# Kernel tuning notes

Measured on AMD Instinct MI355X. Metric: run time of the kernel, lower is better.

Reference implementation:

```python
import jax, jax.numpy as jnp
import numpy as np

B, N, S = 8, 8192, 1024
K = 16          # max_degree
HIDDEN = 192    # hidden_dim, divisible by 2*ndim -> no padding in sincos embed
NDIM = 3
MAX_WAVELENGTH = 10000.0


def sincos_embed(coords, dim, ndim):
    # Continuous sin/cos embedding: dim//ndim channels per coordinate,
    # half sin / half cos, geometric frequencies (UPT-style).
    dpw = dim // ndim                          # dims per coordinate (even)
    ar = jnp.arange(0, dpw, 2, dtype=coords.dtype)
    omega = 1.0 / (MAX_WAVELENGTH ** (ar / dpw))   # (dpw/2,)
    out = coords[..., None] * omega            # (..., ndim, dpw/2)
    emb = jnp.concatenate([jnp.sin(out), jnp.cos(out)], axis=-1)  # (..., ndim, dpw)
    return emb.reshape(*coords.shape[:-1], dim)


def knn_gather(x, sidx, k):
    # x: (B,N,ndim), sidx: (B,S) -> (B,S,k,ndim) coords of k nearest neighbors.
    # Equivalent to the original dense NxN dists[sidx] + argsort[:, :k],
    # but only computes the S rows that are used and uses top_k.
    def per_sample(sx, si):
        sp = sx[si]                                            # (S, ndim)
        d = jnp.sum((sp[:, None, :] - sx[None, :, :]) ** 2, -1)  # (S, N)
        _, nbr = jax.lax.top_k(-d, k)                          # k smallest dists
        return sx[nbr]                                         # (S, k, ndim)
    return jax.vmap(per_sample)(x, sidx)


def setup_inputs() -> dict:
    key = jax.random.key(0)
    ks = jax.random.split(key, 6)
    scale = 0.02
    return {
        "input_points": jax.random.normal(ks[0], (B, N, NDIM), dtype=jnp.float32),
        "supernode_idxs": jax.random.randint(ks[1], (B, S), 0, N),
        "w_in": jax.random.normal(ks[2], (NDIM, HIDDEN), dtype=jnp.float32) * scale,
        "b_in": jnp.zeros((HIDDEN,), dtype=jnp.float32),
        "w1": jax.random.normal(ks[3], (HIDDEN, HIDDEN), dtype=jnp.float32) * scale,
        "b1": jnp.zeros((HIDDEN,), dtype=jnp.float32),
        "w2": jax.random.normal(ks[4], (HIDDEN, HIDDEN), dtype=jnp.float32) * scale,
        "b2": jnp.zeros((HIDDEN,), dtype=jnp.float32),
    }


def reference(input_points, supernode_idxs, w_in, b_in, w1, b1, w2, b2):
    nbr = knn_gather(input_points, supernode_idxs, K)      # (B,S,K,3)
    # input projection + continuous sincos positional embedding
    h = nbr @ w_in + b_in + sincos_embed(nbr, HIDDEN, NDIM)  # (B,S,K,H)
    # message net: Dense -> gelu -> Dense
    h = jax.nn.gelu(h @ w1 + b1)
    h = h @ w2 + b2
    # mean-pool over neighbors per supernode
    return jnp.mean(h, axis=-2)                            # (B,S,H)
```

## Files before the change

kernel.cpp:

```cpp
#include <hip/hip_runtime.h>
#include <stdint.h>

#define NB   8
#define NPTS 8192
#define NS   1024
#define NK   16
#define NH   192
#define KP1  224
#define HROW 232
#define HALF 4096

typedef float    f32x4 __attribute__((ext_vector_type(4)));
typedef short    s16x8 __attribute__((ext_vector_type(8)));
typedef uint32_t u32;
typedef unsigned long long u64;

static __device__ const float OMEGA[32] = {
  1.0f, 0.74989420933245585f, 0.56234132519034907f, 0.42169650342858223f,
  0.31622776601683794f, 0.23713737056616552f, 0.17782794100389229f, 0.13335214321633237f,
  0.1f, 0.074989420933245585f, 0.056234132519034907f, 0.042169650342858223f,
  0.031622776601683794f, 0.023713737056616552f, 0.017782794100389229f, 0.013335214321633237f,
  0.01f, 0.0074989420933245585f, 0.0056234132519034907f, 0.0042169650342858223f,
  0.0031622776601683794f, 0.0023713737056616552f, 0.0017782794100389229f, 0.0013335214321633237f,
  0.001f, 0.00074989420933245585f, 0.00056234132519034907f, 0.00042169650342858223f,
  0.00031622776601683794f, 0.00023713737056616552f, 0.00017782794100389229f, 0.00013335214321633237f };

__device__ __forceinline__ uint16_t f2bf(float f) {
  u32 u = __float_as_uint(f);
  return (uint16_t)((u + 0x7FFFu + ((u >> 16) & 1u)) >> 16);
}

__global__ void __launch_bounds__(64) prep_weights(
    const float* __restrict__ w_in, const float* __restrict__ b_in,
    const float* __restrict__ w1, const float* __restrict__ b1,
    const float* __restrict__ w2,
    uint16_t* __restrict__ wT1e, uint16_t* __restrict__ wT2) {
  const int n = blockIdx.x, t = threadIdx.x;
  float p0 = 0, p1 = 0, p2 = 0, pb = 0;
  #pragma unroll
  for (int kk = 0; kk < 3; ++kk) {
    int c = kk * 64 + t;
    float w1cn = w1[c * NH + n];
    wT1e[n * KP1 + c] = f2bf(w1cn);
    wT2 [n * NH  + c] = f2bf(w2[c * NH + n]);
    p0 = fmaf(w_in[0 * NH + c], w1cn, p0);
    p1 = fmaf(w_in[1 * NH + c], w1cn, p1);
    p2 = fmaf(w_in[2 * NH + c], w1cn, p2);
    pb = fmaf(b_in[c], w1cn, pb);
  }
  #pragma unroll
  for (int off = 32; off; off >>= 1) {
    p0 += __shfl_down(p0, off);
    p1 += __shfl_down(p1, off);
    p2 += __shfl_down(p2, off);
    pb += __shfl_down(pb, off);
  }
  if (t == 0) {
    wT1e[n * KP1 + 192] = f2bf(p0);
    wT1e[n * KP1 + 193] = f2bf(p1);
    wT1e[n * KP1 + 194] = f2bf(p2);
    wT1e[n * KP1 + 195] = f2bf(pb + b1[n]);
  }
  if (t >= 4 && t < 32) wT1e[n * KP1 + 192 + t] = 0;
}

__global__ void __launch_bounds__(512) knn_kernel(const float* __restrict__ pts,
                                                  const int* __restrict__ sidx,
                                                  u64* __restrict__ keys) {
  __shared__ float2 XY[HALF];
  __shared__ float  Zs[HALF];
  const int bid = blockIdx.x;
  const int b = bid >> 6;
  const int chunk = (bid >> 1) & 31;
  const int half = bid & 1;
  const int pbase = half * HALF;
  const float* pb = pts + ((size_t)b * NPTS + pbase) * 3;
  for (int i = threadIdx.x; i < HALF; i += 512) {
    XY[i] = float2{pb[3 * i], pb[3 * i + 1]};
    Zs[i] = pb[3 * i + 2];
  }
  __syncthreads();
  const int wave = threadIdx.x >> 6, lane = threadIdx.x & 63;
  const int sbase = chunk * 32 + wave * 4;

  float sx[4], sy[4], sz[4], minD[4], Td[4];
  u32 minI[4];
  u64 arr[4], T[4];
  #pragma unroll
  for (int q = 0; q < 4; ++q) {
    int si = sidx[b * NS + sbase + q];
    const float* qp = pts + ((size_t)b * NPTS + si) * 3;
    sx[q] = qp[0]; sy[q] = qp[1]; sz[q] = qp[2];
    minD[q] = __uint_as_float(0x7F800000u);
    minI[q] = 0xFFFFFFFFu;
  }

  for (int t = 0; t < HALF / 64; ++t) {
    int lj = t * 64 + lane;
    float2 xy = XY[lj];
    float z = Zs[lj];
    #pragma unroll
    for (int q = 0; q < 4; ++q) {
      float dx = xy.x - sx[q], dy = xy.y - sy[q], dz = z - sz[q];
      float d = __fadd_rn(__fadd_rn(__fmul_rn(dx, dx), __fmul_rn(dy, dy)),
                          __fmul_rn(dz, dz));
      bool c = d < minD[q];
      minD[q] = c ? d : minD[q];
      minI[q] = c ? (u32)(pbase + lj) : minI[q];
    }
  }

  #pragma unroll
  for (int q = 0; q < 4; ++q) {
    u64 key = ((u64)__float_as_uint(minD[q]) << 32) | minI[q];
    #pragma unroll
    for (int k = 2; k <= 64; k <<= 1) {
      #pragma unroll
      for (int jj = k >> 1; jj > 0; jj >>= 1) {
        u64 p = __shfl_xor(key, jj);
        bool up      = ((lane & k) == 0);
        bool lower   = ((lane & jj) == 0);
        bool takeMin = (lower == up);
        bool pLess   = p < key;
        key = (takeMin == pLess) ? p : key;
      }
    }
    arr[q] = (lane < 16) ? key : ~0ull;
    T[q] = __shfl(key, 15);
    Td[q] = __uint_as_float((u32)(T[q] >> 32));
  }

  for (int t = 0; t < HALF / 64; ++t) {
    int lj = t * 64 + lane;
    float2 xy = XY[lj];
    float z = Zs[lj];
    #pragma unroll
    for (int q = 0; q < 4; ++q) {
      float dx = xy.x - sx[q], dy = xy.y - sy[q], dz = z - sz[q];
      float d = __fadd_rn(__fadd_rn(__fmul_rn(dx, dx), __fmul_rn(dy, dy)),
                          __fmul_rn(dz, dz));
      u64 ball = __ballot(d <= Td[q] && (u32)(pbase + lj) != minI[q]);
      if (ball) {
        u64 key = ((u64)__float_as_uint(d) << 32) | (u32)(pbase + lj);
        do {
          int src = __builtin_ctzll(ball);
          ball &= ball - 1;
          u64 k2 = __shfl(key, src);
          if (k2 < T[q]) {
            int r = __popcll(__ballot(arr[q] < k2));
            u64 up = __shfl_up(arr[q], 1);
            if (lane == r) arr[q] = k2;
            else if (lane > r && lane < 16) arr[q] = up;
            T[q] = __shfl(arr[q], 15);
            Td[q] = __uint_as_float((u32)(T[q] >> 32));
          }
        } while (ball);
      }
    }
  }
  #pragma unroll
  for (int q = 0; q < 4; ++q)
    if (lane < 16)
      keys[((size_t)(b * NS + sbase + q)) * 32 + half * 16 + lane] = arr[q];
}

__device__ __forceinline__ float h0ch(int c, const float crd[3]) {
  if (c >= 196) return 0.0f;
  if (c == 195) return 1.0f;
  if (c >= 192) return crd[c - 192];
  int dd = c >> 6, i = c & 63, m = i & 31;
  float arg = crd[dd] * OMEGA[m];
  return (i < 32) ? __sinf(arg) : __cosf(arg);
}

__device__ __forceinline__ float gelu_tanh(float x) {
  float u = 0.7978845608028654f * __fmaf_rn(0.044715f * x, x * x, x);
  float t = 1.0f - 2.0f / (__expf(2.0f * u) + 1.0f);
  return 0.5f * x * (1.0f + t);
}

__global__ void __launch_bounds__(256) mlp_kernel(
    const float* __restrict__ pts, const u64* __restrict__ keys,
    const float* __restrict__ b2v,
    const uint16_t* __restrict__ wT1e, const uint16_t* __restrict__ wT2,
    float* __restrict__ out) {
  __shared__ uint16_t hbuf[128 * HROW];
  __shared__ int nbrL[128];
  const int g = blockIdx.x, tid = threadIdx.x;
  const int wave = tid >> 6, lane = tid & 63;
  const int lrow = lane & 15, lg = lane >> 4;

  {
    int qq = tid >> 5;
    u64 k0 = keys[((size_t)g * 8 + qq) * 32 + (tid & 31)];
    int rank = 0;
    #pragma unroll
    for (int p = 0; p < 32; ++p) {
      u64 other = __shfl(k0, (lane & 32) + p);
      rank += (other < k0);
    }
    if (rank < 16) nbrL[qq * 16 + rank] = (int)(u32)k0;
  }
  __syncthreads();

  {
    int r = tid >> 1, half = tid & 1;
    int grow = g * 128 + r;
    int b = grow >> 14;
    int pidx = nbrL[r];
    const float* pp = pts + ((size_t)b * NPTS + pidx) * 3;
    float crd[3] = {pp[0], pp[1], pp[2]};
    #pragma unroll
    for (int jj = 0; jj < 56; ++jj) {
      int c = half * 112 + jj * 2;
      u32 pk = (u32)f2bf(h0ch(c, crd)) | ((u32)f2bf(h0ch(c + 1, crd)) << 16);
      *(u32*)(hbuf + r * HROW + c) = pk;
    }
  }
  __syncthreads();

  f32x4 acc1[3][8] = {};
  {
    const uint16_t* wbase = wT1e + (size_t)(wave * 48 + lrow) * KP1 + lg * 8;
    uint4 anx[3];
    #pragma unroll
    for (int nt = 0; nt < 3; ++nt) anx[nt] = *(const uint4*)(wbase + nt * 16 * KP1);
    #pragma unroll
    for (int kk = 0; kk < 7; ++kk) {
      uint4 acur[3];
      #pragma unroll
      for (int nt = 0; nt < 3; ++nt) acur[nt] = anx[nt];
      if (kk < 6) {
        #pragma unroll
        for (int nt = 0; nt < 3; ++nt)
          anx[nt] = *(const uint4*)(wbase + nt * 16 * KP1 + (kk + 1) * 32);
      }
      s16x8 bm[8];
      #pragma unroll
      for (int mt = 0; mt < 8; ++mt)
        bm[mt] = __builtin_bit_cast(s16x8,
                   *(const uint4*)(hbuf + (mt * 16 + lrow) * HROW + kk * 32 + lg * 8));
      #pragma unroll
      for (int nt = 0; nt < 3; ++nt)
        #pragma unroll
        for (int mt = 0; mt < 8; ++mt)
          acc1[nt][mt] = __builtin_amdgcn_mfma_f32_16x16x32_bf16(
              __builtin_bit_cast(s16x8, acur[nt]), bm[mt], acc1[nt][mt], 0, 0, 0);
    }
  }
  __syncthreads();

  {
    #pragma unroll
    for (int nt = 0; nt < 3; ++nt) {
      #pragma unroll
      for (int mt = 0; mt < 8; ++mt) {
        u32 lo = (u32)f2bf(gelu_tanh(acc1[nt][mt][0])) |
                 ((u32)f2bf(gelu_tanh(acc1[nt][mt][1])) << 16);
        u32 hi = (u32)f2bf(gelu_tanh(acc1[nt][mt][2])) |
                 ((u32)f2bf(gelu_tanh(acc1[nt][mt][3])) << 16);
        *(uint2*)(hbuf + (mt * 16 + lrow) * HROW + wave * 48 + nt * 16 + lg * 4) =
            uint2{lo, hi};
      }
    }
  }
  __syncthreads();

  f32x4 acc2[8][3] = {};
  {
    const uint16_t* w2base = wT2 + (size_t)(wave * 48 + lrow) * NH + lg * 8;
    uint4 bnx[3];
    #pragma unroll
    for (int nt = 0; nt < 3; ++nt) bnx[nt] = *(const uint4*)(w2base + nt * 16 * NH);
    #pragma unroll
    for (int kk = 0; kk < 6; ++kk) {
      uint4 bcur[3];
      #pragma unroll
      for (int nt = 0; nt < 3; ++nt) bcur[nt] = bnx[nt];
      if (kk < 5) {
        #pragma unroll
        for (int nt = 0; nt < 3; ++nt)
          bnx[nt] = *(const uint4*)(w2base + nt * 16 * NH + (kk + 1) * 32);
      }
      s16x8 am[8];
      #pragma unroll
      for (int mt = 0; mt < 8; ++mt)
        am[mt] = __builtin_bit_cast(s16x8,
                   *(const uint4*)(hbuf + (mt * 16 + lrow) * HROW + kk * 32 + lg * 8));
      #pragma unroll
      for (int mt = 0; mt < 8; ++mt)
        #pragma unroll
        for (int nt = 0; nt < 3; ++nt)
          acc2[mt][nt] = __builtin_amdgcn_mfma_f32_16x16x32_bf16(
              am[mt], __builtin_bit_cast(s16x8, bcur[nt]), acc2[mt][nt], 0, 0, 0);
    }
  }

  {
    #pragma unroll
    for (int mt = 0; mt < 8; ++mt) {
      #pragma unroll
      for (int nt = 0; nt < 3; ++nt) {
        float ssum = acc2[mt][nt][0] + acc2[mt][nt][1] + acc2[mt][nt][2] + acc2[mt][nt][3];
        ssum += __shfl_xor(ssum, 16);
        ssum += __shfl_xor(ssum, 32);
        if (lane < 16) {
          int col = wave * 48 + nt * 16 + lrow;
          out[(size_t)(g * 8 + mt) * NH + col] = ssum * 0.0625f + b2v[col];
        }
      }
    }
  }
}

extern "C" void kernel_launch(void* const* d_in, const int* in_sizes, int n_in,
                              void* d_out, int out_size, void* d_ws, size_t ws_size,
                              hipStream_t stream) {
  (void)in_sizes; (void)n_in; (void)out_size; (void)ws_size;
  const float* pts  = (const float*)d_in[0];
  const int*   sidx = (const int*)d_in[1];
  const float* w_in = (const float*)d_in[2];
  const float* b_in = (const float*)d_in[3];
  const float* w1   = (const float*)d_in[4];
  const float* b1   = (const float*)d_in[5];
  const float* w2   = (const float*)d_in[6];
  const float* b2   = (const float*)d_in[7];
  float* out = (float*)d_out;

  u64* keys = (u64*)d_ws;
  uint16_t* wT1e = (uint16_t*)((char*)d_ws + (size_t)NB * NS * 32 * 8);
  uint16_t* wT2  = wT1e + NH * KP1;

  hipLaunchKernelGGL(prep_weights, dim3(NH), dim3(64), 0, stream,
                     w_in, b_in, w1, b1, w2, wT1e, wT2);

  hipLaunchKernelGGL(knn_kernel, dim3(NB * 64), dim3(512), 0, stream,
                     pts, sidx, keys);

  hipLaunchKernelGGL(mlp_kernel, dim3(NB * NS / 8), dim3(256), 0, stream,
                     pts, keys, b2, wT1e, wT2, out);
}
```

Baseline: 108.5 us.

## Split kNN search into quarters with bitonic merge, cheaper GELU and bf16 packing

The kNN kernel now splits each batch's point set into four quarters instead of two, doubling the grid to 1024 blocks and halving the LDS tile, with a launch-bounds occupancy hint. The MLP kernel then merges four sorted 16-element candidate lists with a bitonic merge network in place of the O(32) rank-counting pass. Separately, GELU is rewritten as x*sigmoid form using a hardware reciprocal, and bf16 conversion uses cheaper round-half-up packing of two values at once. The intent is better load balance and occupancy in kNN plus fewer ALU ops in the MLP, at the cost of doubled key workspace and slightly different rounding.

```diff
diff --git a/kernel.cpp b/kernel.cpp
--- a/kernel.cpp
+++ b/kernel.cpp
@@ -8,7 +8,7 @@
 #define NH   192
 #define KP1  224
 #define HROW 232
-#define HALF 4096
+#define QTR  2048
 
 typedef float    f32x4 __attribute__((ext_vector_type(4)));
 typedef short    s16x8 __attribute__((ext_vector_type(8)));
@@ -29,6 +29,10 @@
   u32 u = __float_as_uint(f);
   return (uint16_t)((u + 0x7FFFu + ((u >> 16) & 1u)) >> 16);
 }
+__device__ __forceinline__ u32 pk2bf(float f0, float f1) {
+  return ((__float_as_uint(f0) + 0x8000u) >> 16) |
+         ((__float_as_uint(f1) + 0x8000u) & 0xFFFF0000u);
+}
 
 __global__ void __launch_bounds__(64) prep_weights(
     const float* __restrict__ w_in, const float* __restrict__ b_in,
@@ -64,18 +68,18 @@
   if (t >= 4 && t < 32) wT1e[n * KP1 + 192 + t] = 0;
 }
 
-__global__ void __launch_bounds__(512) knn_kernel(const float* __restrict__ pts,
-                                                  const int* __restrict__ sidx,
-                                                  u64* __restrict__ keys) {
-  __shared__ float2 XY[HALF];
-  __shared__ float  Zs[HALF];
+__global__ void __launch_bounds__(512, 8) knn_kernel(const float* __restrict__ pts,
+                                                     const int* __restrict__ sidx,
+                                                     u64* __restrict__ keys) {
+  __shared__ float2 XY[QTR];
+  __shared__ float  Zs[QTR];
   const int bid = blockIdx.x;
-  const int b = bid >> 6;
-  const int chunk = (bid >> 1) & 31;
-  const int half = bid & 1;
-  const int pbase = half * HALF;
+  const int b = bid >> 7;
+  const int chunk = (bid >> 2) & 31;
+  const int quarter = bid & 3;
+  const int pbase = quarter * QTR;
   const float* pb = pts + ((size_t)b * NPTS + pbase) * 3;
-  for (int i = threadIdx.x; i < HALF; i += 512) {
+  for (int i = threadIdx.x; i < QTR; i += 512) {
     XY[i] = float2{pb[3 * i], pb[3 * i + 1]};
     Zs[i] = pb[3 * i + 2];
   }
@@ -95,7 +99,7 @@
     minI[q] = 0xFFFFFFFFu;
   }
 
-  for (int t = 0; t < HALF / 64; ++t) {
+  for (int t = 0; t < QTR / 64; ++t) {
     int lj = t * 64 + lane;
     float2 xy = XY[lj];
     float z = Zs[lj];
@@ -118,11 +122,8 @@
       #pragma unroll
       for (int jj = k >> 1; jj > 0; jj >>= 1) {
         u64 p = __shfl_xor(key, jj);
-        bool up      = ((lane & k) == 0);
-        bool lower   = ((lane & jj) == 0);
-        bool takeMin = (lower == up);
-        bool pLess   = p < key;
-        key = (takeMin == pLess) ? p : key;
+        bool takeMin = (((lane & jj) == 0) == ((lane & k) == 0));
+        key = (takeMin == (p < key)) ? p : key;
       }
     }
     arr[q] = (lane < 16) ? key : ~0ull;
@@ -130,7 +131,7 @@
     Td[q] = __uint_as_float((u32)(T[q] >> 32));
   }
 
-  for (int t = 0; t < HALF / 64; ++t) {
+  for (int t = 0; t < QTR / 64; ++t) {
     int lj = t * 64 + lane;
     float2 xy = XY[lj];
     float z = Zs[lj];
@@ -161,7 +162,7 @@
   #pragma unroll
   for (int q = 0; q < 4; ++q)
     if (lane < 16)
-      keys[((size_t)(b * NS + sbase + q)) * 32 + half * 16 + lane] = arr[q];
+      keys[((size_t)(b * NS + sbase + q)) * 64 + quarter * 16 + lane] = arr[q];
 }
 
 __device__ __forceinline__ float h0ch(int c, const float crd[3]) {
@@ -173,10 +174,9 @@
   return (i < 32) ? __sinf(arg) : __cosf(arg);
 }
 
-__device__ __forceinline__ float gelu_tanh(float x) {
-  float u = 0.7978845608028654f * __fmaf_rn(0.044715f * x, x * x, x);
-  float t = 1.0f - 2.0f / (__expf(2.0f * u) + 1.0f);
-  return 0.5f * x * (1.0f + t);
+__device__ __forceinline__ float gelu_f(float x) {
+  float v = -1.5957691216057308f * __fmaf_rn(0.044715f * x, x * x, x);
+  return x * __builtin_amdgcn_rcpf(1.0f + __expf(v));
 }
 
 __global__ void __launch_bounds__(256) mlp_kernel(
@@ -190,16 +190,25 @@
   const int wave = tid >> 6, lane = tid & 63;
   const int lrow = lane & 15, lg = lane >> 4;
 
-  {
-    int qq = tid >> 5;
-    u64 k0 = keys[((size_t)g * 8 + qq) * 32 + (tid & 31)];
-    int rank = 0;
-    #pragma unroll
-    for (int p = 0; p < 32; ++p) {
-      u64 other = __shfl(k0, (lane & 32) + p);
-      rank += (other < k0);
-    }
-    if (rank < 16) nbrL[qq * 16 + rank] = (int)(u32)k0;
+  #pragma unroll
+  for (int ii = 0; ii < 2; ++ii) {
+    int q = ii * 4 + wave;
+    int list = lane >> 4, pos = lane & 15;
+    int rpos = (list & 1) ? (15 - pos) : pos;
+    u64 key = keys[((size_t)g * 8 + q) * 64 + list * 16 + rpos];
+    #pragma unroll
+    for (int jj = 16; jj > 0; jj >>= 1) {
+      u64 p = __shfl_xor(key, jj);
+      bool takeMin = (((lane & jj) == 0) == ((lane & 32) == 0));
+      key = (takeMin == (p < key)) ? p : key;
+    }
+    #pragma unroll
+    for (int jj = 32; jj > 0; jj >>= 1) {
+      u64 p = __shfl_xor(key, jj);
+      bool takeMin = ((lane & jj) == 0);
+      key = (takeMin == (p < key)) ? p : key;
+    }
+    if (lane < 16) nbrL[q * 16 + lane] = (int)(u32)key;
   }
   __syncthreads();
 
@@ -211,10 +220,12 @@
     const float* pp = pts + ((size_t)b * NPTS + pidx) * 3;
     float crd[3] = {pp[0], pp[1], pp[2]};
     #pragma unroll
-    for (int jj = 0; jj < 56; ++jj) {
-      int c = half * 112 + jj * 2;
-      u32 pk = (u32)f2bf(h0ch(c, crd)) | ((u32)f2bf(h0ch(c + 1, crd)) << 16);
-      *(u32*)(hbuf + r * HROW + c) = pk;
+    for (int jj = 0; jj < 28; ++jj) {
+      int c = half * 112 + jj * 4;
+      uint2 pk;
+      pk.x = pk2bf(h0ch(c, crd),     h0ch(c + 1, crd));
+      pk.y = pk2bf(h0ch(c + 2, crd), h0ch(c + 3, crd));
+      *(uint2*)(hbuf + r * HROW + c) = pk;
     }
   }
   __syncthreads();
@@ -255,12 +266,10 @@
     for (int nt = 0; nt < 3; ++nt) {
       #pragma unroll
       for (int mt = 0; mt < 8; ++mt) {
-        u32 lo = (u32)f2bf(gelu_tanh(acc1[nt][mt][0])) |
-                 ((u32)f2bf(gelu_tanh(acc1[nt][mt][1])) << 16);
-        u32 hi = (u32)f2bf(gelu_tanh(acc1[nt][mt][2])) |
-                 ((u32)f2bf(gelu_tanh(acc1[nt][mt][3])) << 16);
-        *(uint2*)(hbuf + (mt * 16 + lrow) * HROW + wave * 48 + nt * 16 + lg * 4) =
-            uint2{lo, hi};
+        uint2 pk;
+        pk.x = pk2bf(gelu_f(acc1[nt][mt][0]), gelu_f(acc1[nt][mt][1]));
+        pk.y = pk2bf(gelu_f(acc1[nt][mt][2]), gelu_f(acc1[nt][mt][3]));
+        *(uint2*)(hbuf + (mt * 16 + lrow) * HROW + wave * 48 + nt * 16 + lg * 4) = pk;
       }
     }
   }
@@ -328,13 +337,13 @@
   float* out = (float*)d_out;
 
   u64* keys = (u64*)d_ws;
-  uint16_t* wT1e = (uint16_t*)((char*)d_ws + (size_t)NB * NS * 32 * 8);
+  uint16_t* wT1e = (uint16_t*)((char*)d_ws + (size_t)NB * NS * 64 * 8);
   uint16_t* wT2  = wT1e + NH * KP1;
 
   hipLaunchKernelGGL(prep_weights, dim3(NH), dim3(64), 0, stream,
                      w_in, b_in, w1, b1, w2, wT1e, wT2);
 
-  hipLaunchKernelGGL(knn_kernel, dim3(NB * 64), dim3(512), 0, stream,
+  hipLaunchKernelGGL(knn_kernel, dim3(NB * 128), dim3(512), 0, stream,
                      pts, sidx, keys);
 
   hipLaunchKernelGGL(mlp_kernel, dim3(NB * NS / 8), dim3(256), 0, stream,
```

Measured after the change: 95.24 us. 1.14x faster.
